# Kernel tuning notes

Hardware: AMD Instinct MI355X
Metric: run time of the kernel (lower is better)

## Reference

```python
import jax, jax.numpy as jnp
import numpy as np

TAU = 0.5  # config.tau -> ContrastiveLoss temperature


def setup_inputs() -> dict:
    key = jax.random.key(0)
    k1, _ = jax.random.split(key)
    last_hidden_states = jax.random.normal(k1, (256, 512, 768), dtype=jnp.float32)
    input_mask = jnp.ones((256, 512), dtype=jnp.float32)
    return {"last_hidden_states": last_hidden_states, "input_mask": input_mask}


def reference(last_hidden_states, input_mask):
    # --- get_bert_emb with pooling == 'mean' (faithful: sums WITHOUT masking,
    # divides by mask.sum, exactly as the torch code does) ---
    pooled = last_hidden_states.sum(axis=1) / input_mask.sum(axis=-1, keepdims=True)  # [B, H]

    # --- ContrastiveLoss (NT-Xent style, vectorized form of the double loop) ---
    # z = F.normalize(emb_in, dim=1); cosine similarity of normalized rows == z @ z.T
    z = pooled / jnp.linalg.norm(pooled, axis=1, keepdims=True)  # [B, H]
    logits = (z @ z.T) / TAU  # [B, B] similarity_matrix / temperature

    B = logits.shape[0]
    n = B // 4

    # denominator_i = sum_{k != i} exp(S[i,k]/tau)  -> log-domain with diagonal masked
    diag = jnp.eye(B, dtype=bool)
    logden = jax.nn.logsumexp(jnp.where(diag, -jnp.inf, logits), axis=1)  # [B]

    # loss_ij = -log(exp(S[i,j]/tau) / denom_i) = logden[i] - logits[i,j], summed over i<j<n
    pair_mask = jnp.triu(jnp.ones((n, n), dtype=bool), k=1)
    per_pair = logden[:n, None] - logits[:n, :n]  # [n, n]
    total = jnp.sum(jnp.where(pair_mask, per_pair, jnp.zeros_like(per_pair)))

    # final scaling exactly as in the torch code: -2/n * (n-1) * loss
    return -2.0 / n * (n - 1) * total
```

## Files before the change

### kernel.cpp

```cpp
#include <hip/hip_runtime.h>
#include <math.h>

#define B 256
#define S 512
#define H 768
#define H4 (H / 4)
#define NSMALL 64

__device__ __forceinline__ float waveReduceSum(float v) {
    v += __shfl_down(v, 32);
    v += __shfl_down(v, 16);
    v += __shfl_down(v, 8);
    v += __shfl_down(v, 4);
    v += __shfl_down(v, 2);
    v += __shfl_down(v, 1);
    return v;
}

__global__ void pool_z_k(const float* __restrict__ lhs,
                         const float* __restrict__ mask,
                         float* __restrict__ z) {
    const int b = blockIdx.x;
    const int t = threadIdx.x;
    const int col = t % H4;
    const int rg  = t / H4;

    __shared__ float4 red[3][H4];
    __shared__ float sm[12];
    __shared__ float sq[3];

    const float4* __restrict__ src =
        reinterpret_cast<const float4*>(lhs) + (size_t)b * S * H4;
    float4 acc = make_float4(0.f, 0.f, 0.f, 0.f);
#pragma unroll 8
    for (int s = 0; s < S / 4; ++s) {
        float4 v = src[(size_t)(4 * s + rg) * H4 + col];
        acc.x += v.x; acc.y += v.y; acc.z += v.z; acc.w += v.w;
    }
    if (rg > 0) red[rg - 1][col] = acc;

    float mv = (t < S) ? mask[(size_t)b * S + t] : 0.f;
    float w = waveReduceSum(mv);
    if ((t & 63) == 0) sm[t >> 6] = w;
    __syncthreads();

    float msum = 0.f;
#pragma unroll
    for (int k = 0; k < 12; ++k) msum += sm[k];

    float4 p = acc;
    if (rg == 0) {
        float4 r0 = red[0][col], r1 = red[1][col], r2 = red[2][col];
        p.x += r0.x + r1.x + r2.x;
        p.y += r0.y + r1.y + r2.y;
        p.z += r0.z + r1.z + r2.z;
        p.w += r0.w + r1.w + r2.w;
        const float inv_m = 1.0f / msum;
        p.x *= inv_m; p.y *= inv_m; p.z *= inv_m; p.w *= inv_m;
        float s2 = p.x * p.x + p.y * p.y + p.z * p.z + p.w * p.w;
        float ws2 = waveReduceSum(s2);
        if ((t & 63) == 0) sq[t >> 6] = ws2;
    }
    __syncthreads();
    if (rg == 0) {
        const float inv_n = 1.0f / sqrtf(sq[0] + sq[1] + sq[2]);
        float4 zp = make_float4(p.x * inv_n, p.y * inv_n, p.z * inv_n, p.w * inv_n);
        reinterpret_cast<float4*>(z + (size_t)b * H)[col] = zp;
    }
}

__global__ void row_part_k(const float* __restrict__ z,
                           float* __restrict__ sp,
                           float* __restrict__ pairneg) {
    const int i  = blockIdx.x >> 2;
    const int jc = blockIdx.x & 3;
    const int t  = threadIdx.x;
    const int col = t & 63;
    const int q   = t >> 6;
    const int j   = jc * 64 + col;

    __shared__ float zi[H];
    __shared__ float pd[4][64];

    zi[t]       = z[(size_t)i * H + t];
    zi[t + 256] = z[(size_t)i * H + 256 + t];
    zi[t + 512] = z[(size_t)i * H + 512 + t];
    __syncthreads();

    const float4* __restrict__ zj4 =
        reinterpret_cast<const float4*>(z + (size_t)j * H) + q * 48;
    const float4* zi4 = reinterpret_cast<const float4*>(zi) + q * 48;
    float d0 = 0.f, d1 = 0.f;
#pragma unroll 8
    for (int k = 0; k < 48; k += 2) {
        float4 a  = zi4[k];     float4 c1 = zj4[k];
        float4 a2 = zi4[k + 1]; float4 c2 = zj4[k + 1];
        d0 += a.x * c1.x + a.y * c1.y + a.z * c1.z + a.w * c1.w;
        d1 += a2.x * c2.x + a2.y * c2.y + a2.z * c2.z + a2.w * c2.w;
    }
    pd[q][col] = d0 + d1;
    __syncthreads();

    if (t < 64) {
        const float dot = pd[0][col] + pd[1][col] + pd[2][col] + pd[3][col];
        const float logit = dot * 2.0f;
        const float ev = (j == i) ? 0.f : expf(logit);
        float s = waveReduceSum(ev);
        if (col == 0) sp[i * 4 + jc] = s;
        if (jc == 0) {
            const float term = (col > i) ? -logit : 0.f;
            float ts = waveReduceSum(term);
            if (col == 0) pairneg[i] = ts;
        }
    }
}

__global__ void final_k(const float* __restrict__ sp,
                        const float* __restrict__ pairneg,
                        float* __restrict__ out) {
    const int i = threadIdx.x;
    const float s = sp[i * 4] + sp[i * 4 + 1] + sp[i * 4 + 2] + sp[i * 4 + 3];
    const float logden = logf(s);
    const float row = (float)(NSMALL - 1 - i) * logden + pairneg[i];
    float tot = waveReduceSum(row);
    if (i == 0) {
        out[0] = (-2.0f / (float)NSMALL) * (float)(NSMALL - 1) * tot;
    }
}

extern "C" void kernel_launch(void* const* d_in, const int* in_sizes, int n_in,
                              void* d_out, int out_size, void* d_ws, size_t ws_size,
                              hipStream_t stream) {
    const float* lhs  = (const float*)d_in[0];
    const float* mask = (const float*)d_in[1];
    float* out = (float*)d_out;
    float* ws  = (float*)d_ws;

    float* z       = ws;
    float* sp      = z + (size_t)B * H;
    float* pairneg = sp + NSMALL * 4;

    pool_z_k<<<B, H, 0, stream>>>(lhs, mask, z);
    row_part_k<<<NSMALL * 4, 256, 0, stream>>>(z, sp, pairneg);
    final_k<<<1, 64, 0, stream>>>(sp, pairneg, out);
}
```

Measured before the change: 84.97 us.

## Fuse pooling, similarity and final reduction into one cooperative kernel

Result: slower. 144.8 us (+70.4%).

```diff
diff --git a/kernel.cpp b/kernel.cpp
--- a/kernel.cpp
+++ b/kernel.cpp
@@ -1,5 +1,8 @@
 #include <hip/hip_runtime.h>
+#include <hip/hip_cooperative_groups.h>
 #include <math.h>
+
+namespace cg = cooperative_groups;
 
 #define B 256
 #define S 512
@@ -17,114 +20,123 @@
     return v;
 }
 
-__global__ void pool_z_k(const float* __restrict__ lhs,
-                         const float* __restrict__ mask,
-                         float* __restrict__ z) {
-    const int b = blockIdx.x;
-    const int t = threadIdx.x;
-    const int col = t % H4;
-    const int rg  = t / H4;
+__global__ void __launch_bounds__(768) fused_k(const float* __restrict__ lhs,
+                                               const float* __restrict__ mask,
+                                               float* __restrict__ z,
+                                               float* __restrict__ sp,
+                                               float* __restrict__ pairneg,
+                                               float* __restrict__ out) {
+    cg::grid_group grid = cg::this_grid();
+    const int blk = blockIdx.x;
+    const int t   = threadIdx.x;
 
-    __shared__ float4 red[3][H4];
-    __shared__ float sm[12];
-    __shared__ float sq[3];
+    __shared__ __align__(16) float smem[2320];
 
-    const float4* __restrict__ src =
-        reinterpret_cast<const float4*>(lhs) + (size_t)b * S * H4;
-    float4 acc = make_float4(0.f, 0.f, 0.f, 0.f);
+    {
+        const int col = t % H4;
+        const int rg  = t / H4;
+        float4* red = reinterpret_cast<float4*>(smem);
+        float*  sm  = smem + 3 * H4 * 4;
+        float*  sq  = sm + 12;
+
+        const float4* __restrict__ src =
+            reinterpret_cast<const float4*>(lhs) + (size_t)blk * S * H4;
+        float4 acc = make_float4(0.f, 0.f, 0.f, 0.f);
 #pragma unroll 8
-    for (int s = 0; s < S / 4; ++s) {
-        float4 v = src[(size_t)(4 * s + rg) * H4 + col];
-        acc.x += v.x; acc.y += v.y; acc.z += v.z; acc.w += v.w;
-    }
-    if (rg > 0) red[rg - 1][col] = acc;
+        for (int s = 0; s < S / 4; ++s) {
+            float4 v = src[(size_t)(4 * s + rg) * H4 + col];
+            acc.x += v.x; acc.y += v.y; acc.z += v.z; acc.w += v.w;
+        }
+        if (rg > 0) red[(rg - 1) * H4 + col] = acc;
 
-    float mv = (t < S) ? mask[(size_t)b * S + t] : 0.f;
-    float w = waveReduceSum(mv);
-    if ((t & 63) == 0) sm[t >> 6] = w;
-    __syncthreads();
+        float mv = (t < S) ? mask[(size_t)blk * S + t] : 0.f;
+        float w = waveReduceSum(mv);
+        if ((t & 63) == 0) sm[t >> 6] = w;
+        __syncthreads();
 
-    float msum = 0.f;
+        float msum = 0.f;
 #pragma unroll
-    for (int k = 0; k < 12; ++k) msum += sm[k];
+        for (int k = 0; k < 12; ++k) msum += sm[k];
 
-    float4 p = acc;
-    if (rg == 0) {
-        float4 r0 = red[0][col], r1 = red[1][col], r2 = red[2][col];
-        p.x += r0.x + r1.x + r2.x;
-        p.y += r0.y + r1.y + r2.y;
-        p.z += r0.z + r1.z + r2.z;
-        p.w += r0.w + r1.w + r2.w;
-        const float inv_m = 1.0f / msum;
-        p.x *= inv_m; p.y *= inv_m; p.z *= inv_m; p.w *= inv_m;
-        float s2 = p.x * p.x + p.y * p.y + p.z * p.z + p.w * p.w;
-        float ws2 = waveReduceSum(s2);
-        if ((t & 63) == 0) sq[t >> 6] = ws2;
-    }
-    __syncthreads();
-    if (rg == 0) {
-        const float inv_n = 1.0f / sqrtf(sq[0] + sq[1] + sq[2]);
-        float4 zp = make_float4(p.x * inv_n, p.y * inv_n, p.z * inv_n, p.w * inv_n);
-        reinterpret_cast<float4*>(z + (size_t)b * H)[col] = zp;
-    }
-}
-
-__global__ void row_part_k(const float* __restrict__ z,
-                           float* __restrict__ sp,
-                           float* __restrict__ pairneg) {
-    const int i  = blockIdx.x >> 2;
-    const int jc = blockIdx.x & 3;
-    const int t  = threadIdx.x;
-    const int col = t & 63;
-    const int q   = t >> 6;
-    const int j   = jc * 64 + col;
-
-    __shared__ float zi[H];
-    __shared__ float pd[4][64];
-
-    zi[t]       = z[(size_t)i * H + t];
-    zi[t + 256] = z[(size_t)i * H + 256 + t];
-    zi[t + 512] = z[(size_t)i * H + 512 + t];
-    __syncthreads();
-
-    const float4* __restrict__ zj4 =
-        reinterpret_cast<const float4*>(z + (size_t)j * H) + q * 48;
-    const float4* zi4 = reinterpret_cast<const float4*>(zi) + q * 48;
-    float d0 = 0.f, d1 = 0.f;
-#pragma unroll 8
-    for (int k = 0; k < 48; k += 2) {
-        float4 a  = zi4[k];     float4 c1 = zj4[k];
-        float4 a2 = zi4[k + 1]; float4 c2 = zj4[k + 1];
-        d0 += a.x * c1.x + a.y * c1.y + a.z * c1.z + a.w * c1.w;
-        d1 += a2.x * c2.x + a2.y * c2.y + a2.z * c2.z + a2.w * c2.w;
-    }
-    pd[q][col] = d0 + d1;
-    __syncthreads();
-
-    if (t < 64) {
-        const float dot = pd[0][col] + pd[1][col] + pd[2][col] + pd[3][col];
-        const float logit = dot * 2.0f;
-        const float ev = (j == i) ? 0.f : expf(logit);
-        float s = waveReduceSum(ev);
-        if (col == 0) sp[i * 4 + jc] = s;
-        if (jc == 0) {
-            const float term = (col > i) ? -logit : 0.f;
-            float ts = waveReduceSum(term);
-            if (col == 0) pairneg[i] = ts;
+        float4 p = acc;
+        if (rg == 0) {
+            float4 r0 = red[0 * H4 + col];
+            float4 r1 = red[1 * H4 + col];
+            float4 r2 = red[2 * H4 + col];
+            p.x += r0.x + r1.x + r2.x;
+            p.y += r0.y + r1.y + r2.y;
+            p.z += r0.z + r1.z + r2.z;
+            p.w += r0.w + r1.w + r2.w;
+            const float inv_m = 1.0f / msum;
+            p.x *= inv_m; p.y *= inv_m; p.z *= inv_m; p.w *= inv_m;
+            float s2 = p.x * p.x + p.y * p.y + p.z * p.z + p.w * p.w;
+            float ws2 = waveReduceSum(s2);
+            if ((t & 63) == 0) sq[t >> 6] = ws2;
+        }
+        __syncthreads();
+        if (rg == 0) {
+            const float inv_n = 1.0f / sqrtf(sq[0] + sq[1] + sq[2]);
+            float4 zp = make_float4(p.x * inv_n, p.y * inv_n,
+                                    p.z * inv_n, p.w * inv_n);
+            reinterpret_cast<float4*>(z + (size_t)blk * H)[col] = zp;
         }
     }
-}
 
-__global__ void final_k(const float* __restrict__ sp,
-                        const float* __restrict__ pairneg,
-                        float* __restrict__ out) {
-    const int i = threadIdx.x;
-    const float s = sp[i * 4] + sp[i * 4 + 1] + sp[i * 4 + 2] + sp[i * 4 + 3];
-    const float logden = logf(s);
-    const float row = (float)(NSMALL - 1 - i) * logden + pairneg[i];
-    float tot = waveReduceSum(row);
-    if (i == 0) {
-        out[0] = (-2.0f / (float)NSMALL) * (float)(NSMALL - 1) * tot;
+    grid.sync();
+
+    {
+        const int i   = blk >> 2;
+        const int jc  = blk & 3;
+        const int col = t & 63;
+        const int q   = t >> 6;
+        const int j   = jc * 64 + col;
+
+        float* zi = smem;
+        float* pd = smem + H;
+
+        zi[t] = z[(size_t)i * H + t];
+        __syncthreads();
+
+        const float4* __restrict__ zj4 =
+            reinterpret_cast<const float4*>(z + (size_t)j * H) + q * 16;
+        const float4* zi4 = reinterpret_cast<const float4*>(zi) + q * 16;
+        float d0 = 0.f, d1 = 0.f;
+#pragma unroll
+        for (int k = 0; k < 16; k += 2) {
+            float4 a  = zi4[k];     float4 c1 = zj4[k];
+            float4 a2 = zi4[k + 1]; float4 c2 = zj4[k + 1];
+            d0 += a.x * c1.x + a.y * c1.y + a.z * c1.z + a.w * c1.w;
+            d1 += a2.x * c2.x + a2.y * c2.y + a2.z * c2.z + a2.w * c2.w;
+        }
+        pd[q * 64 + col] = d0 + d1;
+        __syncthreads();
+
+        if (t < 64) {
+            float dot = 0.f;
+#pragma unroll
+            for (int q2 = 0; q2 < 12; ++q2) dot += pd[q2 * 64 + t];
+            const float logit = dot * 2.0f;
+            const float ev = (j == i) ? 0.f : expf(logit);
+            float s = waveReduceSum(ev);
+            if (t == 0) sp[i * 4 + jc] = s;
+            if (jc == 0) {
+                const float term = (t > i) ? -logit : 0.f;
+                float ts = waveReduceSum(term);
+                if (t == 0) pairneg[i] = ts;
+            }
+        }
+    }
+
+    grid.sync();
+
+    if (blk == 0 && t < 64) {
+        const int i = t;
+        const float s = sp[i * 4] + sp[i * 4 + 1] + sp[i * 4 + 2] + sp[i * 4 + 3];
+        const float row = (float)(NSMALL - 1 - i) * logf(s) + pairneg[i];
+        float tot = waveReduceSum(row);
+        if (t == 0) {
+            out[0] = (-2.0f / (float)NSMALL) * (float)(NSMALL - 1) * tot;
+        }
     }
 }
 
@@ -140,7 +152,8 @@
     float* sp      = z + (size_t)B * H;
     float* pairneg = sp + NSMALL * 4;
 
-    pool_z_k<<<B, H, 0, stream>>>(lhs, mask, z);
-    row_part_k<<<NSMALL * 4, 256, 0, stream>>>(z, sp, pairneg);
-    final_k<<<1, 64, 0, stream>>>(sp, pairneg, out);
+    void* args[] = { (void*)&lhs, (void*)&mask, (void*)&z,
+                     (void*)&sp, (void*)&pairneg, (void*)&out };
+    hipLaunchCooperativeKernel(reinterpret_cast<void*>(fused_k),
+                               dim3(B), dim3(H), args, 0, stream);
 }
```
